# Optimization experiments

Measured on AMD Instinct MI355X. Metric: run time of the kernel, lower is better.

Reference implementation:

```python
import jax, jax.numpy as jnp
from jax import lax
import numpy as np

GRID = 64
MAP = 15000.0
SCALE = MAP / GRID  # 234.375
R = int(1100 / SCALE)  # 4
SIGMA = 1.5
C = 16
B = 768
N_KILL = 49152
N_TRAIL = 393216

TOWERS = np.array([(8955, 8510), (9767, 10113), (11134, 11207), (11593, 11669), (13052, 12612), (12611, 13084), (5846, 6396), (5048, 4812), (3651, 3696), (3210, 3217), (2177, 1807), (1748, 2270), (4318, 13875), (981, 10441), (7943, 13411), (1512, 6699), (1169, 4287), (1172, 3583), (10481, 13650), (11275, 13657), (11275, 13663), (13866, 4505), (10504, 1029), (13327, 8226), (13624, 10572), (6919, 1483), (13599, 11319), (4281, 1253), (3468, 1230), (13594, 11319)], dtype=np.float32)

# ---- static buffers (numpy, computed once at import) ----
_tg = np.clip((TOWERS / SCALE).astype(np.int64), 0, GRID - 1)
TX, TY = _tg[:, 0], _tg[:, 1]
_xs = np.arange(GRID)
# per-tower coverage disc on the full canvas: equivalent to clipped range_mask placement
DISC = (((_xs[None, None, :] - TX[:, None, None]) ** 2 + (_xs[None, :, None] - TY[:, None, None]) ** 2) <= R * R).astype(np.float32)  # [30, H, W]
_ks = int(2 * 4 * SIGMA + 1)
if _ks % 2 == 0:
    _ks += 1
_x = (np.arange(_ks) - _ks // 2).astype(np.float32)
_k1 = np.exp(-_x ** 2 / (2 * SIGMA ** 2))
_k2 = np.outer(_k1, _k1)
_k2 = _k2 / _k2.sum()
KERNEL = np.broadcast_to(_k2, (C, 1, _ks, _ks)).astype(np.float32).copy()  # depthwise OIHW
PAD = _ks // 2
DRAG_X, DRAG_Y = int(10000.0 / SCALE), int(5000.0 / SCALE)   # (42, 21)
BARON_X, BARON_Y = int(5000.0 / SCALE), int(10000.0 / SCALE)  # (21, 42)


def _to_grid(coords):
    return jnp.clip((coords / SCALE).astype(jnp.int32), 0, GRID - 1)


def setup_inputs() -> dict:
    key = jax.random.key(0)
    ks = jax.random.split(key, 10)
    return {
        "player_coords": jax.random.uniform(ks[0], (N_TRAIL, 2), jnp.float32) * MAP,
        "player_vals": jax.random.uniform(ks[1], (N_TRAIL,), jnp.float32),
        "dead_towers_mask": jax.random.uniform(ks[2], (B, 30), jnp.float32),
        "kill_coords": jax.random.uniform(ks[3], (N_KILL, 2), jnp.float32) * MAP,
        "kill_vals": jax.random.uniform(ks[4], (N_KILL,), jnp.float32),
        "obj_status": jax.random.uniform(ks[5], (B, 2), jnp.float32),
        "player_b_idx": jax.random.randint(ks[6], (N_TRAIL,), 0, B, jnp.int32),
        "player_channels": jax.random.randint(ks[7], (N_TRAIL,), 0, 10, jnp.int32),
        "kill_teams": jax.random.randint(ks[8], (N_KILL,), 0, 2, jnp.int32),
        "kill_b_idx": jax.random.randint(ks[9], (N_KILL,), 0, B, jnp.int32),
    }


def reference(player_coords, player_vals, dead_towers_mask, kill_coords, kill_vals, obj_status, player_b_idx, player_channels, kill_teams, kill_b_idx):
    b = dead_towers_mask.shape[0]
    dead = dead_towers_mask > 0.5          # [B, 30]
    alive_f = (~dead).astype(jnp.float32)
    dead_f = dead.astype(jnp.float32)

    # channels 0/1: alive/dead tower markers (idempotent set -> scatter-max)
    ch0 = jnp.zeros((b, GRID, GRID), jnp.float32).at[:, TY, TX].max(alive_f)
    ch1 = jnp.zeros((b, GRID, GRID), jnp.float32).at[:, TY, TX].max(dead_f)

    # channel 2: max of binary range discs over alive towers == any-coverage indicator
    cov = alive_f @ jnp.asarray(DISC).reshape(30, -1)  # [B, H*W]
    ch2 = (cov > 0).astype(jnp.float32).reshape(b, GRID, GRID)

    # channel 3: objective markers
    ch3 = (jnp.zeros((b, GRID, GRID), jnp.float32)
           .at[:, DRAG_Y, DRAG_X].set((obj_status[:, 0] > 0.5).astype(jnp.float32))
           .at[:, BARON_Y, BARON_X].set((obj_status[:, 1] > 0.5).astype(jnp.float32)))

    canvas = jnp.concatenate(
        [ch0[:, None], ch1[:, None], ch2[:, None], ch3[:, None],
         jnp.zeros((b, C - 4, GRID, GRID), jnp.float32)], axis=1)  # [B, 16, H, W]

    # kill events: scatter-add into channels 4 + team
    kg = _to_grid(kill_coords)
    canvas = canvas.at[kill_b_idx, 4 + kill_teams, kg[:, 1], kg[:, 0]].add(kill_vals)

    # player trails: scatter-add into channels 6 + player_channel
    pg = _to_grid(player_coords)
    canvas = canvas.at[player_b_idx, 6 + player_channels, pg[:, 1], pg[:, 0]].add(player_vals)

    # depthwise gaussian blur
    blurred = lax.conv_general_dilated(
        canvas, jnp.asarray(KERNEL),
        window_strides=(1, 1), padding=[(PAD, PAD), (PAD, PAD)],
        feature_group_count=C,
        dimension_numbers=("NCHW", "OIHW", "NCHW"))
    return blurred
```

## Files before the change

### kernel.cpp

```cpp
#include <hip/hip_runtime.h>
#include <string.h>

#define GRID    64
#define BATCH   768
#define C       16
#define NT      30
#define N_KILL  49152
#define N_TRAIL 393216
#define CELLS   4096
#define IMG     (C * CELLS)
#define SCALE   234.375f
#define NSC     12
#define NIMG    (BATCH * NSC)
#define CAPI    128
#define TRS     65
#define TRWORDS (GRID * TRS)
#define TRVEC   (TRWORDS / 4)

__device__ constexpr int TXc[NT] = {38,41,47,49,55,53,24,21,15,13, 9, 7,18, 4,33, 6, 4, 5,44,48,48,59,44,56,58,29,58,18,14,58};
__device__ constexpr int TYc[NT] = {36,43,47,49,53,55,27,20,15,13, 7, 9,59,44,57,28,18,15,58,58,58,19, 4,35,45, 6,48, 5, 5,48};

__device__ constexpr float W13[13] = {
    8.92216e-05f, 1.02820e-03f, 7.59741e-03f, 3.59943e-02f, 1.09341e-01f,
    2.12968e-01f, 2.65964e-01f, 2.12968e-01f, 1.09341e-01f, 3.59943e-02f,
    7.59741e-03f, 1.02820e-03f, 8.92216e-05f};

__global__ __launch_bounds__(256) void zero_counts(unsigned* __restrict__ counts) {
    const int gid = blockIdx.x * 256 + threadIdx.x;
    if (gid < NIMG) counts[gid] = 0;
}

__global__ __launch_bounds__(256) void bin_points(
    const float* __restrict__ kc, const float* __restrict__ kv,
    const int*   __restrict__ kt, const int*   __restrict__ kb,
    const float* __restrict__ pc, const float* __restrict__ pv,
    const int*   __restrict__ pb, const int*   __restrict__ pch,
    unsigned* __restrict__ counts, unsigned* __restrict__ recs)
{
    const int gid = blockIdx.x * 256 + threadIdx.x;
    int img, gx, gy; float val;
    if (gid < N_KILL) {
        const int i = gid;
        const float2 xy = ((const float2*)kc)[i];
        gx = min(max((int)(xy.x / SCALE), 0), GRID - 1);
        gy = min(max((int)(xy.y / SCALE), 0), GRID - 1);
        val = kv[i];
        img = kb[i] * NSC + kt[i];
    } else {
        const int i = gid - N_KILL;
        const float2 xy = ((const float2*)pc)[i];
        gx = min(max((int)(xy.x / SCALE), 0), GRID - 1);
        gy = min(max((int)(xy.y / SCALE), 0), GRID - 1);
        val = pv[i];
        img = pb[i] * NSC + 2 + pch[i];
    }
    _Float16 h = (_Float16)val;
    unsigned short us;
    memcpy(&us, &h, 2);
    const unsigned rec = ((unsigned)(gy * GRID + gx) << 16) | (unsigned)us;
    const unsigned slot = atomicAdd(&counts[img], 1u);
    if (slot < CAPI) recs[(size_t)img * CAPI + slot] = rec;
}

template<bool BINS>
__global__ __launch_bounds__(64) void fused_blur(
    const float* __restrict__ dead_mask,
    const float* __restrict__ obj_status,
    const unsigned* __restrict__ counts,
    const unsigned* __restrict__ recs,
    const float* canvas,
    float* __restrict__ out)
{
    const int t  = threadIdx.x;
    const int bc = blockIdx.x;
    const int b  = bc >> 4;
    const int c  = bc & 15;
    const size_t base = (size_t)bc * CELLS;

    __shared__ __align__(16) float s_tr[TRWORDS];
    __shared__ float s_alive[NT];

    if (c < 4 && t < NT) s_alive[t] = (dead_mask[b * NT + t] > 0.5f) ? 0.0f : 1.0f;

    const bool dense = (c == 2) || (!BINS && c >= 4);

    if (dense) {
        __syncthreads();
        float r[76];
        #pragma unroll
        for (int i = 0; i < 76; ++i) r[i] = 0.0f;

        if (c == 2) {
            unsigned long long mask = 0ULL;
            #pragma unroll
            for (int i = 0; i < NT; ++i) {
                const int dy  = t - TYc[i];
                const int ady = dy < 0 ? -dy : dy;
                if (ady <= 4 && s_alive[i] > 0.0f) {
                    const int hw = (ady == 0) ? 4 : (ady <= 2) ? 3 : (ady == 3) ? 2 : 0;
                    int lo = TXc[i] - hw; if (lo < 0)  lo = 0;
                    int hi = TXc[i] + hw; if (hi > 63) hi = 63;
                    mask |= (((1ULL << (hi - lo + 1)) - 1ULL) << lo);
                }
            }
            #pragma unroll
            for (int x = 0; x < GRID; ++x) r[6 + x] = (float)((mask >> x) & 1ULL);
        } else {
            #pragma unroll
            for (int k = 0; k < 16; ++k) {
                const float4 v = ((const float4*)(canvas + base))[t * 16 + k];
                r[6 + 4*k + 0] = v.x; r[6 + 4*k + 1] = v.y;
                r[6 + 4*k + 2] = v.z; r[6 + 4*k + 3] = v.w;
            }
        }
        #pragma unroll
        for (int x = 0; x < GRID; ++x) {
            float acc = 0.0f;
            #pragma unroll
            for (int d = 0; d < 13; ++d) acc = fmaf(W13[d], r[x + d], acc);
            s_tr[x * TRS + t] = acc;
        }
        __syncthreads();
    } else {
        const float4 z = make_float4(0.f, 0.f, 0.f, 0.f);
        #pragma unroll
        for (int i = 0; i < 17; ++i) {
            const int idx = i * 64 + t;
            if (idx < TRVEC) ((float4*)s_tr)[idx] = z;
        }
        __syncthreads();

        int n; size_t ibase = 0;
        float obj0 = 0.f, obj1 = 0.f;
        if (BINS && c >= 4) {
            const int img = b * NSC + (c - 4);
            n = (int)counts[img];
            if (n > CAPI) n = CAPI;
            ibase = (size_t)img * CAPI;
        } else {
            n = NT + 2;
            if (c == 3) {
                obj0 = obj_status[b * 2 + 0];
                obj1 = obj_status[b * 2 + 1];
            }
        }

        float wlane = 0.f;
        #pragma unroll
        for (int j = 0; j < 13; ++j) if (t == j) wlane = W13[j];

        const int ntaps = n * 13;
        for (int k0 = 0; k0 < ntaps; k0 += 64) {
            const int k = k0 + t;
            int i = (int)((unsigned)k / 13u);
            const int dd = k - i * 13;
            if (i > n - 1) i = n - 1;

            int gx, gy; float val;
            if (BINS && c >= 4) {
                const unsigned rec = recs[ibase + i];
                const int cell = (int)(rec >> 16);
                gx = cell & 63; gy = cell >> 6;
                const unsigned short us = (unsigned short)(rec & 0xFFFFu);
                _Float16 h;
                memcpy(&h, &us, 2);
                val = (float)h;
            } else {
                if (i < NT) {
                    gx = TXc[i]; gy = TYc[i];
                    const float a = s_alive[i];
                    if (c == 0) {
                        val = (i == 20 || i == 29) ? 0.f
                            : (i == 19) ? fmaxf(a, s_alive[20])
                            : (i == 26) ? fmaxf(a, s_alive[29]) : a;
                    } else if (c == 1) {
                        val = (i == 20 || i == 29) ? 0.f
                            : (i == 19) ? fmaxf(1.f - a, 1.f - s_alive[20])
                            : (i == 26) ? fmaxf(1.f - a, 1.f - s_alive[29])
                            : 1.f - a;
                    } else {
                        val = 0.f;
                    }
                } else if (c == 3) {
                    if (i == NT) { gx = 42; gy = 21; val = (obj0 > 0.5f) ? 1.f : 0.f; }
                    else         { gx = 21; gy = 42; val = (obj1 > 0.5f) ? 1.f : 0.f; }
                } else {
                    gx = 0; gy = 0; val = 0.f;
                }
            }

            const float w  = __shfl(wlane, dd);
            const int   xl = gx - 6 + dd;
            if (k < ntaps && (unsigned)xl < 64u && val != 0.f)
                atomicAdd(&s_tr[xl * TRS + gy], val * w);
        }
        __syncthreads();
    }

    float v[76];
    #pragma unroll
    for (int i = 0; i < 6; ++i) { v[i] = 0.0f; v[70 + i] = 0.0f; }
    #pragma unroll
    for (int k = 0; k < GRID; ++k) v[6 + k] = s_tr[t * TRS + k];

    #pragma unroll
    for (int y = 0; y < GRID; ++y) {
        float acc = 0.0f;
        #pragma unroll
        for (int d = 0; d < 13; ++d) acc = fmaf(W13[d], v[y + d], acc);
        __builtin_nontemporal_store(acc, &out[base + y * GRID + t]);
    }
}

__global__ __launch_bounds__(256) void zero12(float* __restrict__ out) {
    const int j = blockIdx.x;
    const int b = j / NSC, ch = 4 + j % NSC;
    float4* p = (float4*)(out + (size_t)(b * C + ch) * CELLS);
    #pragma unroll
    for (int k = 0; k < 4; ++k) p[k * 256 + threadIdx.x] = make_float4(0.f,0.f,0.f,0.f);
}

__global__ __launch_bounds__(256) void scatter_global(
    const float* __restrict__ kc, const float* __restrict__ kv,
    const int*   __restrict__ kt, const int*   __restrict__ kb,
    const float* __restrict__ pc, const float* __restrict__ pv,
    const int*   __restrict__ pb, const int*   __restrict__ pch,
    float* __restrict__ out)
{
    const int gid = blockIdx.x * 256 + threadIdx.x;
    if (gid < N_KILL) {
        const int i = gid;
        const int gx = min(max((int)(kc[2*i]   / SCALE), 0), GRID - 1);
        const int gy = min(max((int)(kc[2*i+1] / SCALE), 0), GRID - 1);
        atomicAdd(out + (size_t)kb[i]*IMG + (4+kt[i])*CELLS + gy*GRID + gx, kv[i]);
    } else {
        const int i = gid - N_KILL;
        const int gx = min(max((int)(pc[2*i]   / SCALE), 0), GRID - 1);
        const int gy = min(max((int)(pc[2*i+1] / SCALE), 0), GRID - 1);
        atomicAdd(out + (size_t)pb[i]*IMG + (6+pch[i])*CELLS + gy*GRID + gx, pv[i]);
    }
}

extern "C" void kernel_launch(void* const* d_in, const int* in_sizes, int n_in,
                              void* d_out, int out_size, void* d_ws, size_t ws_size,
                              hipStream_t stream)
{
    const float* player_coords = (const float*)d_in[0];
    const float* player_vals   = (const float*)d_in[1];
    const float* dead_mask     = (const float*)d_in[2];
    const float* kill_coords   = (const float*)d_in[3];
    const float* kill_vals     = (const float*)d_in[4];
    const float* obj_status    = (const float*)d_in[5];
    const int*   player_b      = (const int*)d_in[6];
    const int*   player_ch     = (const int*)d_in[7];
    const int*   kill_teams    = (const int*)d_in[8];
    const int*   kill_b        = (const int*)d_in[9];
    float* out = (float*)d_out;

    const size_t counts_bytes = (size_t)NIMG * sizeof(unsigned);
    const size_t recs_bytes   = (size_t)NIMG * CAPI * sizeof(unsigned);
    const int n_scatter_blocks = (N_KILL + N_TRAIL) / 256;

    if (ws_size >= counts_bytes + recs_bytes) {
        unsigned* counts = (unsigned*)d_ws;
        unsigned* recs   = (unsigned*)((char*)d_ws + counts_bytes);
        zero_counts<<<(NIMG + 255) / 256, 256, 0, stream>>>(counts);
        bin_points<<<n_scatter_blocks, 256, 0, stream>>>(
            kill_coords, kill_vals, kill_teams, kill_b,
            player_coords, player_vals, player_b, player_ch,
            counts, recs);
        fused_blur<true><<<BATCH * C, 64, 0, stream>>>(
            dead_mask, obj_status, counts, recs, nullptr, out);
    } else {
        zero12<<<NIMG, 256, 0, stream>>>(out);
        scatter_global<<<n_scatter_blocks, 256, 0, stream>>>(
            kill_coords, kill_vals, kill_teams, kill_b,
            player_coords, player_vals, player_b, player_ch, out);
        fused_blur<false><<<BATCH * C, 64, 0, stream>>>(
            dead_mask, obj_status, nullptr, nullptr, out, out);
    }
}
```

Before: 104.1 us.

## Split blur across 256 threads per image with padded row-major shared tile

Raises the fused blur block from 64 to 256 threads. Each wavefront now handles a 16-row or 16-column strip with a 28-element halo, where before each thread carried a full 76-element register line. The shared intermediate becomes a zero-padded row-major tile, so the vertical pass needs no boundary checks. Per-channel tower and objective values are precomputed once in shared memory. The aim is to cut register pressure, raise occupancy and parallelise the scatter taps, at the cost of redundant halo work, extra barriers, and dropping the nontemporal stores.

```diff
diff --git a/kernel.cpp b/kernel.cpp
--- a/kernel.cpp
+++ b/kernel.cpp
@@ -13,9 +13,9 @@
 #define NSC     12
 #define NIMG    (BATCH * NSC)
 #define CAPI    128
-#define TRS     65
-#define TRWORDS (GRID * TRS)
-#define TRVEC   (TRWORDS / 4)
+#define STR     65
+#define ROWS    76
+#define HWORDS  (ROWS * STR)
 
 __device__ constexpr int TXc[NT] = {38,41,47,49,55,53,24,21,15,13, 9, 7,18, 4,33, 6, 4, 5,44,48,48,59,44,56,58,29,58,18,14,58};
 __device__ constexpr int TYc[NT] = {36,43,47,49,53,55,27,20,15,13, 7, 9,59,44,57,28,18,15,58,58,58,19, 4,35,45, 6,48, 5, 5,48};
@@ -63,7 +63,7 @@
 }
 
 template<bool BINS>
-__global__ __launch_bounds__(64) void fused_blur(
+__global__ __launch_bounds__(256) void fused_blur(
     const float* __restrict__ dead_mask,
     const float* __restrict__ obj_status,
     const unsigned* __restrict__ counts,
@@ -76,25 +76,51 @@
     const int b  = bc >> 4;
     const int c  = bc & 15;
     const size_t base = (size_t)bc * CELLS;
-
-    __shared__ __align__(16) float s_tr[TRWORDS];
+    const int u = t & 63, q = t >> 6;
+
+    __shared__ __align__(16) float s_h[HWORDS];
     __shared__ float s_alive[NT];
-
-    if (c < 4 && t < NT) s_alive[t] = (dead_mask[b * NT + t] > 0.5f) ? 0.0f : 1.0f;
-
-    const bool dense = (c == 2) || (!BINS && c >= 4);
-
-    if (dense) {
-        __syncthreads();
-        float r[76];
-        #pragma unroll
-        for (int i = 0; i < 76; ++i) r[i] = 0.0f;
-
+    __shared__ float s_w[13];
+    __shared__ float s_vval[32];
+
+    float4* z4 = (float4*)s_h;
+    const float4 z = make_float4(0.f, 0.f, 0.f, 0.f);
+    #pragma unroll
+    for (int i = 0; i < 5; ++i) {
+        const int idx = i * 256 + t;
+        if (idx < HWORDS / 4) z4[idx] = z;
+    }
+    if (t < 13) s_w[t] = W13[t];
+    if (t < NT) s_alive[t] = (dead_mask[b * NT + t] > 0.5f) ? 0.0f : 1.0f;
+    __syncthreads();
+
+    if (c < 4 && c != 2 && t < 32) {
+        float val = 0.f;
+        if (t < NT) {
+            const float a = s_alive[t];
+            if (c == 0)
+                val = (t == 20 || t == 29) ? 0.f
+                    : (t == 19) ? fmaxf(a, s_alive[20])
+                    : (t == 26) ? fmaxf(a, s_alive[29]) : a;
+            else if (c == 1)
+                val = (t == 20 || t == 29) ? 0.f
+                    : (t == 19) ? fmaxf(1.f - a, 1.f - s_alive[20])
+                    : (t == 26) ? fmaxf(1.f - a, 1.f - s_alive[29])
+                    : 1.f - a;
+        } else if (c == 3) {
+            val = (obj_status[b * 2 + (t - NT)] > 0.5f) ? 1.f : 0.f;
+        }
+        s_vval[t] = val;
+    }
+    __syncthreads();
+
+    if (c == 2 || (!BINS && c >= 4)) {
+        float w28[28];
         if (c == 2) {
             unsigned long long mask = 0ULL;
             #pragma unroll
             for (int i = 0; i < NT; ++i) {
-                const int dy  = t - TYc[i];
+                const int dy  = u - TYc[i];
                 const int ady = dy < 0 ? -dy : dy;
                 if (ady <= 4 && s_alive[i] > 0.0f) {
                     const int hw = (ady == 0) ? 4 : (ady <= 2) ? 3 : (ady == 3) ? 2 : 0;
@@ -104,111 +130,73 @@
                 }
             }
             #pragma unroll
-            for (int x = 0; x < GRID; ++x) r[6 + x] = (float)((mask >> x) & 1ULL);
+            for (int k = 0; k < 28; ++k) {
+                const int col = 16 * q - 6 + k;
+                w28[k] = ((unsigned)col < 64u) ? (float)((mask >> col) & 1ULL) : 0.f;
+            }
         } else {
             #pragma unroll
-            for (int k = 0; k < 16; ++k) {
-                const float4 v = ((const float4*)(canvas + base))[t * 16 + k];
-                r[6 + 4*k + 0] = v.x; r[6 + 4*k + 1] = v.y;
-                r[6 + 4*k + 2] = v.z; r[6 + 4*k + 3] = v.w;
+            for (int k = 0; k < 28; ++k) {
+                const int col = 16 * q - 6 + k;
+                w28[k] = ((unsigned)col < 64u) ? canvas[base + u * GRID + col] : 0.f;
             }
         }
         #pragma unroll
-        for (int x = 0; x < GRID; ++x) {
-            float acc = 0.0f;
-            #pragma unroll
-            for (int d = 0; d < 13; ++d) acc = fmaf(W13[d], r[x + d], acc);
-            s_tr[x * TRS + t] = acc;
-        }
-        __syncthreads();
-    } else {
-        const float4 z = make_float4(0.f, 0.f, 0.f, 0.f);
-        #pragma unroll
-        for (int i = 0; i < 17; ++i) {
-            const int idx = i * 64 + t;
-            if (idx < TRVEC) ((float4*)s_tr)[idx] = z;
-        }
-        __syncthreads();
-
+        for (int j = 0; j < 16; ++j) {
+            float acc = 0.f;
+            #pragma unroll
+            for (int d = 0; d < 13; ++d) acc = fmaf(W13[d], w28[j + d], acc);
+            s_h[(6 + u) * STR + 16 * q + j] = acc;
+        }
+    } else {
         int n; size_t ibase = 0;
-        float obj0 = 0.f, obj1 = 0.f;
-        if (BINS && c >= 4) {
+        if (c >= 4) {
             const int img = b * NSC + (c - 4);
             n = (int)counts[img];
             if (n > CAPI) n = CAPI;
             ibase = (size_t)img * CAPI;
         } else {
-            n = NT + 2;
-            if (c == 3) {
-                obj0 = obj_status[b * 2 + 0];
-                obj1 = obj_status[b * 2 + 1];
-            }
-        }
-
-        float wlane = 0.f;
-        #pragma unroll
-        for (int j = 0; j < 13; ++j) if (t == j) wlane = W13[j];
-
+            n = 32;
+        }
         const int ntaps = n * 13;
-        for (int k0 = 0; k0 < ntaps; k0 += 64) {
+        for (int k0 = 0; k0 < ntaps; k0 += 256) {
             const int k = k0 + t;
             int i = (int)((unsigned)k / 13u);
             const int dd = k - i * 13;
+            const bool valid = (k < ntaps);
             if (i > n - 1) i = n - 1;
 
             int gx, gy; float val;
-            if (BINS && c >= 4) {
+            if (c >= 4) {
                 const unsigned rec = recs[ibase + i];
-                const int cell = (int)(rec >> 16);
-                gx = cell & 63; gy = cell >> 6;
-                const unsigned short us = (unsigned short)(rec & 0xFFFFu);
+                gx = (int)((rec >> 16) & 63u);
+                gy = (int)(rec >> 22);
+                unsigned short us = (unsigned short)(rec & 0xFFFFu);
                 _Float16 h;
                 memcpy(&h, &us, 2);
                 val = (float)h;
             } else {
-                if (i < NT) {
-                    gx = TXc[i]; gy = TYc[i];
-                    const float a = s_alive[i];
-                    if (c == 0) {
-                        val = (i == 20 || i == 29) ? 0.f
-                            : (i == 19) ? fmaxf(a, s_alive[20])
-                            : (i == 26) ? fmaxf(a, s_alive[29]) : a;
-                    } else if (c == 1) {
-                        val = (i == 20 || i == 29) ? 0.f
-                            : (i == 19) ? fmaxf(1.f - a, 1.f - s_alive[20])
-                            : (i == 26) ? fmaxf(1.f - a, 1.f - s_alive[29])
-                            : 1.f - a;
-                    } else {
-                        val = 0.f;
-                    }
-                } else if (c == 3) {
-                    if (i == NT) { gx = 42; gy = 21; val = (obj0 > 0.5f) ? 1.f : 0.f; }
-                    else         { gx = 21; gy = 42; val = (obj1 > 0.5f) ? 1.f : 0.f; }
-                } else {
-                    gx = 0; gy = 0; val = 0.f;
-                }
-            }
-
-            const float w  = __shfl(wlane, dd);
+                gx = (i < NT) ? TXc[i] : ((i == NT) ? 42 : 21);
+                gy = (i < NT) ? TYc[i] : ((i == NT) ? 21 : 42);
+                val = s_vval[i];
+            }
             const int   xl = gx - 6 + dd;
-            if (k < ntaps && (unsigned)xl < 64u && val != 0.f)
-                atomicAdd(&s_tr[xl * TRS + gy], val * w);
-        }
-        __syncthreads();
-    }
-
-    float v[76];
-    #pragma unroll
-    for (int i = 0; i < 6; ++i) { v[i] = 0.0f; v[70 + i] = 0.0f; }
-    #pragma unroll
-    for (int k = 0; k < GRID; ++k) v[6 + k] = s_tr[t * TRS + k];
-
-    #pragma unroll
-    for (int y = 0; y < GRID; ++y) {
-        float acc = 0.0f;
+            const float wv = s_w[dd] * val;
+            if (valid && (unsigned)xl < 64u && val != 0.f)
+                atomicAdd(&s_h[(6 + gy) * STR + xl], wv);
+        }
+    }
+    __syncthreads();
+
+    float v[28];
+    #pragma unroll
+    for (int k = 0; k < 28; ++k) v[k] = s_h[(16 * q + k) * STR + u];
+    #pragma unroll
+    for (int j = 0; j < 16; ++j) {
+        float acc = 0.f;
         #pragma unroll
-        for (int d = 0; d < 13; ++d) acc = fmaf(W13[d], v[y + d], acc);
-        __builtin_nontemporal_store(acc, &out[base + y * GRID + t]);
+        for (int d = 0; d < 13; ++d) acc = fmaf(W13[d], v[j + d], acc);
+        out[base + (16 * q + j) * GRID + u] = acc;
     }
 }
 
@@ -269,14 +257,14 @@
             kill_coords, kill_vals, kill_teams, kill_b,
             player_coords, player_vals, player_b, player_ch,
             counts, recs);
-        fused_blur<true><<<BATCH * C, 64, 0, stream>>>(
+        fused_blur<true><<<BATCH * C, 256, 0, stream>>>(
             dead_mask, obj_status, counts, recs, nullptr, out);
     } else {
         zero12<<<NIMG, 256, 0, stream>>>(out);
         scatter_global<<<n_scatter_blocks, 256, 0, stream>>>(
             kill_coords, kill_vals, kill_teams, kill_b,
             player_coords, player_vals, player_b, player_ch, out);
-        fused_blur<false><<<BATCH * C, 64, 0, stream>>>(
+        fused_blur<false><<<BATCH * C, 256, 0, stream>>>(
             dead_mask, obj_status, nullptr, nullptr, out, out);
     }
 }
```

Measured after the change: 102.3 us. About the same (-1.7%).
